# Performance work log

Measured on AMD Instinct MI355X. Metric: run time of the kernel, lower is better.

## Reference

```python
import jax, jax.numpy as jnp
import numpy as np

K = 1.0            # curvature (manifold.k); sqrt(K)=1 simplifies formulas
EPS = 1e-5         # module eps used in variance rescale
MIN_NORM = 1e-8    # clamp for sqrt of Lorentz inners
MAX_EUCLID = 10.0  # rescale_to_max_euclid cap (keeps cosh/sinh in fp32 range)


def l_inner(x, y):
    # Lorentz inner product <x,y>_L = -x0*y0 + <x_s, y_s>, keepdim
    return -x[..., :1] * y[..., :1] + jnp.sum(x[..., 1:] * y[..., 1:], axis=-1, keepdims=True)


def centroid(x):
    # Lorentzian centroid over the group axis (dim=-2)
    avg = jnp.mean(x, axis=-2, keepdims=True)
    denom = jnp.sqrt(jnp.clip(-l_inner(avg, avg), MIN_NORM, None))
    return avg / denom


def logmap(x, y):
    alpha = jnp.clip(-l_inner(x, y), 1.0 + 1e-7, None)   # -<x,y>_L >= 1
    dist = jnp.arccosh(alpha)
    nomin = y - alpha * x                                # y + <x,y>_L * x
    denom = jnp.sqrt(jnp.clip(l_inner(nomin, nomin), MIN_NORM, None))
    return dist * nomin / denom


def _plus_origin(p):
    # p + o where o = (1, 0, ..., 0)
    return jnp.concatenate([p[..., :1] + 1.0, p[..., 1:]], axis=-1)


def transp0back(x, v):
    # parallel transport of tangent v at x back to the origin o
    nom = -v[..., :1]                 # <o, v>_L = -v0
    denom = 1.0 + x[..., :1]          # K - <x, o>_L = 1 + x0
    return v + (nom / denom) * _plus_origin(x)


def transp0(y, v):
    # parallel transport of tangent v at origin o to point y
    nom = l_inner(y, v)
    denom = 1.0 + y[..., :1]          # K - <o, y>_L = 1 + y0
    return v + (nom / denom) * _plus_origin(y)


def rescale_to_max_euclid(u):
    n = jnp.linalg.norm(u, axis=-1, keepdims=True)
    scale = jnp.minimum(1.0, MAX_EUCLID / jnp.clip(n, MIN_NORM, None))
    return u * scale


def expmap(x, u):
    nrm = jnp.sqrt(jnp.clip(l_inner(u, u), MIN_NORM, None))
    return jnp.cosh(nrm) * x + jnp.sinh(nrm) * (u / nrm)


def setup_inputs() -> dict:
    key = jax.random.key(0)
    k1, = jax.random.split(key, 1)
    bs, h, w, c = 64, 56, 56, 128
    # sample spatial components, lift onto the hyperboloid: x0 = sqrt(1+|xs|^2)
    xs = 0.5 * jax.random.normal(k1, (bs, h, w, c - 1), dtype=jnp.float32)
    x0 = jnp.sqrt(1.0 + jnp.sum(xs * xs, axis=-1, keepdims=True))
    x = jnp.concatenate([x0, xs], axis=-1)
    gamma = jnp.ones((c,), dtype=jnp.float32)
    # beta = manifold.origin(c) = (1, 0, ..., 0)
    beta = jnp.zeros((c,), dtype=jnp.float32).at[0].set(1.0)
    return {"x": x, "gamma": gamma, "beta": beta, "groups": 8}


def reference(x, gamma, beta, groups):
    bs, h, w, c = x.shape
    xg = x.reshape(bs, -1, groups, c)                    # (bs, hw/g, g, c)
    mean = centroid(xg)                                  # (bs, hw/g, 1, c)
    x_T = logmap(mean, xg)                               # tangent at mean
    x_T = transp0back(mean, x_T)                         # tangent at origin
    # Frechet-style variance: mean Euclidean norm over spatial dim (dim=1)
    var = jnp.mean(jnp.linalg.norm(x_T, axis=-1, keepdims=True), axis=1, keepdims=True)
    x_T = x_T * (gamma / (var + EPS))
    x_T = rescale_to_max_euclid(x_T)
    x_T = transp0(beta, x_T)                             # transport to beta
    out = expmap(beta, x_T)
    return out.reshape(bs, h, w, c)
```

## Files before the change

### kernel.cpp

```cpp
#include <hip/hip_runtime.h>
#include <math.h>


constexpr int S_GROUPS = 392;
constexpr int N_GROUPS = 64 * S_GROUPS;

__device__ __forceinline__ void wave_lds_fence() {
  __asm__ volatile("" ::: "memory");
  __builtin_amdgcn_wave_barrier();
  __asm__ volatile("" ::: "memory");
}

__device__ __forceinline__ void rsum8x3(float& a, float& b, float& c) {
#pragma unroll
  for (int m = 1; m <= 4; m <<= 1) {
    a += __shfl_xor(a, m, 64);
    b += __shfl_xor(b, m, 64);
    c += __shfl_xor(c, m, 64);
  }
}

__device__ __forceinline__ void fold_mean(const float v[16], int lane,
                                          float& c0, float& c1) {
  float a8[8];
  const bool h5 = (lane & 32) != 0;
#pragma unroll
  for (int i = 0; i < 8; ++i) {
    float kp = h5 ? v[i + 8] : v[i];
    float sd = h5 ? v[i] : v[i + 8];
    a8[i] = kp + __shfl_xor(sd, 32, 64);
  }
  float a4[4];
  const bool h4 = (lane & 16) != 0;
#pragma unroll
  for (int i = 0; i < 4; ++i) {
    float kp = h4 ? a8[i + 4] : a8[i];
    float sd = h4 ? a8[i] : a8[i + 4];
    a4[i] = kp + __shfl_xor(sd, 16, 64);
  }
  const bool h3 = (lane & 8) != 0;
  float kp0 = h3 ? a4[2] : a4[0], sd0 = h3 ? a4[0] : a4[2];
  float kp1 = h3 ? a4[3] : a4[1], sd1 = h3 ? a4[1] : a4[3];
  c0 = (kp0 + __shfl_xor(sd0, 8, 64)) * 0.125f;
  c1 = (kp1 + __shfl_xor(sd1, 8, 64)) * 0.125f;
}

struct CoreOut {
  float avg[16];
  float sc, k, coef;
  float iaL, dpL, yyE, y0p, avg0;
};

__device__ __forceinline__ void core(const float v[16], int lane,
                                     float* __restrict__ smrow, CoreOut& o) {
  const int p = lane >> 3, q = lane & 7;
  float c0, c1;
  fold_mean(v, lane, c0, c1);
  *reinterpret_cast<float2*>(&smrow[q * 16 + p * 2]) = make_float2(c0, c1);
  wave_lds_fence();
#pragma unroll
  for (int j = 0; j < 4; ++j)
    *reinterpret_cast<float4*>(&o.avg[4 * j]) =
        *reinterpret_cast<const float4*>(&smrow[q * 16 + 4 * j]);
  wave_lds_fence();

  float pa = 0.f, pd = 0.f, py = 0.f;
#pragma unroll
  for (int i = 0; i < 16; ++i) {
    pa = fmaf(o.avg[i], o.avg[i], pa);
    pd = fmaf(o.avg[i], v[i], pd);
    py = fmaf(v[i], v[i], py);
  }
  if (q == 0) {
    pa -= 2.f * o.avg[0] * o.avg[0];
    pd -= 2.f * o.avg[0] * v[0];
  }
  rsum8x3(pa, pd, py);
  o.iaL = pa;
  o.dpL = pd;
  o.yyE = py;
  o.y0p = __shfl(v[0], lane & 56, 64);
  o.avg0 = __shfl(o.avg[0], 0, 64);

  float rden = rsqrtf(fmaxf(-pa, 1e-8f));
  float a_raw = -pd * rden;
  float alpha = fmaxf(a_raw, 1.f + 1e-7f);
  float t = alpha - 1.f;
  float dist = log1pf(t + sqrtf(t * (alpha + 1.f)));
  float yyL = py - 2.f * o.y0p * o.y0p;
  float inn = fmaxf(yyL + 2.f * alpha * a_raw - alpha * alpha, 1e-8f);
  o.sc = dist * rsqrtf(inn);
  float am = alpha * rden;
  float mean0 = rden * o.avg0;
  float v0 = o.sc * (o.y0p - am * o.avg0);
  o.coef = -v0 / (1.f + mean0);
  o.k = o.coef * rden - o.sc * am;
}

__device__ __forceinline__ float xt_norm(const CoreOut& A) {
  float yavgE = A.dpL + 2.f * A.avg0 * A.y0p;
  float aaE = A.iaL + 2.f * A.avg0 * A.avg0;
  float nsq = A.sc * A.sc * A.yyE + A.k * A.k * aaE + 2.f * A.sc * A.k * yavgE +
              A.coef * A.coef + 2.f * A.coef * (A.sc * A.y0p + A.k * A.avg0);
  return sqrtf(fmaxf(nsq, 0.f));
}

__global__ __launch_bounds__(256) void lngn_pass1(const float* __restrict__ x,
                                                  float* __restrict__ var_part) {
  __shared__ float sm[4][2][128];
  const int w = threadIdx.x >> 6, lane = threadIdx.x & 63;
  const int p = lane >> 3, q = lane & 7;
  const int wid0 = (blockIdx.x * 4 + w) * 2;
  const float* b0 = x + (size_t)wid0 * 1024 + p * 128 + q * 16;
  float vA[16], vB[16];
#pragma unroll
  for (int j = 0; j < 4; ++j) {
    *reinterpret_cast<float4*>(&vA[4 * j]) =
        *reinterpret_cast<const float4*>(b0 + 4 * j);
    *reinterpret_cast<float4*>(&vB[4 * j]) =
        *reinterpret_cast<const float4*>(b0 + 1024 + 4 * j);
  }
  CoreOut A, B;
  core(vA, lane, sm[w][0], A);
  core(vB, lane, sm[w][1], B);
  float nA = xt_norm(A), nB = xt_norm(B);
  if (q == 0) {
    var_part[(size_t)wid0 * 8 + p] = nA;
    var_part[(size_t)(wid0 + 1) * 8 + p] = nB;
  }
}

__global__ __launch_bounds__(256) void lngn_finalize(
    const float* __restrict__ var_part, float* __restrict__ var_out) {
  const int wv = (int)((blockIdx.x * 256 + threadIdx.x) >> 6);
  const int lane = threadIdx.x & 63;
  const int b = wv >> 3, p = wv & 7;
  const float* base = var_part + (size_t)b * S_GROUPS * 8 + p;
  float s = 0.f;
  for (int s0 = lane; s0 < S_GROUPS; s0 += 64) s += base[(size_t)s0 * 8];
#pragma unroll
  for (int m = 32; m >= 1; m >>= 1) s += __shfl_xor(s, m, 64);
  if (lane == 0) var_out[wv] = s * (1.f / (float)S_GROUPS);
}

__global__ __launch_bounds__(256) void lngn_pass2(
    const float* __restrict__ x, const float* __restrict__ gamma,
    const float* __restrict__ beta, const float* __restrict__ var,
    float* __restrict__ out) {
  __shared__ float sm[4][128];
  const int w = threadIdx.x >> 6, lane = threadIdx.x & 63;
  const int p = lane >> 3, q = lane & 7;
  const int wid = blockIdx.x * 4 + w;
  const size_t base = (size_t)wid * 1024 + p * 128 + q * 16;
  float v[16];
#pragma unroll
  for (int j = 0; j < 4; ++j)
    *reinterpret_cast<float4*>(&v[4 * j]) =
        *reinterpret_cast<const float4*>(x + base + 4 * j);
  CoreOut C;
  core(v, lane, sm[w], C);

  const int b = wid / S_GROUPS;
  const float s1 = 1.f / (var[b * 8 + p] + 1e-5f);
  float gm[16], bt[16];
#pragma unroll
  for (int j = 0; j < 4; ++j) {
    *reinterpret_cast<float4*>(&gm[4 * j]) =
        *reinterpret_cast<const float4*>(gamma + q * 16 + 4 * j);
    *reinterpret_cast<float4*>(&bt[4 * j]) =
        *reinterpret_cast<const float4*>(beta + q * 16 + 4 * j);
  }

  float u[16];
  float pe = 0.f, pb = 0.f, pbb = 0.f;
#pragma unroll
  for (int i = 0; i < 16; ++i) {
    float xt = fmaf(C.sc, v[i], C.k * C.avg[i]);
    if (i == 0) xt += (q == 0) ? C.coef : 0.f;
    u[i] = xt * (gm[i] * s1);
    pe = fmaf(u[i], u[i], pe);
    pb = fmaf(bt[i], u[i], pb);
    pbb = fmaf(bt[i], bt[i], pbb);
  }
  if (q == 0) {
    pb -= 2.f * bt[0] * u[0];
    pbb -= 2.f * bt[0] * bt[0];
  }
  rsum8x3(pe, pb, pbb);
  const float u0 = __shfl(u[0], 0, 64);
  const float bt0 = __shfl(bt[0], 0, 64);

  float n = sqrtf(pe);
  float scl = fminf(1.f, 10.f / fmaxf(n, 1e-8f));
  float c2 = scl * pb / (1.f + bt0);
  float uuL = pe - 2.f * u0 * u0;
  float innw = scl * scl * uuL + 2.f * scl * c2 * (pb - u0) +
               c2 * c2 * (pbb - 2.f * bt0 - 1.f);
  float nrm = sqrtf(fmaxf(innw, 1e-8f));
  float e = expf(nrm), ie = 1.f / e;
  float chv = 0.5f * (e + ie);
  float isn = (0.5f * (e - ie)) / nrm;
  float C1 = chv + isn * c2, C2 = isn * scl, C3 = isn * c2;
  float o16[16];
#pragma unroll
  for (int i = 0; i < 16; ++i) o16[i] = fmaf(C1, bt[i], C2 * u[i]);
  if (q == 0) o16[0] += C3;
  float* ob = out + base;
#pragma unroll
  for (int j = 0; j < 4; ++j)
    *reinterpret_cast<float4*>(ob + 4 * j) =
        *reinterpret_cast<const float4*>(&o16[4 * j]);
}

extern "C" void kernel_launch(void* const* d_in, const int* in_sizes, int n_in,
                              void* d_out, int out_size, void* d_ws,
                              size_t ws_size, hipStream_t stream) {
  const float* x = (const float*)d_in[0];
  const float* gamma = (const float*)d_in[1];
  const float* beta = (const float*)d_in[2];
  float* out = (float*)d_out;
  float* var_part = (float*)d_ws;
  float* var_final = var_part + (size_t)N_GROUPS * 8;

  lngn_pass1<<<N_GROUPS / 8, 256, 0, stream>>>(x, var_part);
  lngn_finalize<<<128, 256, 0, stream>>>(var_part, var_final);
  lngn_pass2<<<N_GROUPS / 4, 256, 0, stream>>>(x, gamma, beta, var_final, out);
}
```

Measured before the change: 224.4 us.

## Cache per-group centroid and coefficients in pass 1; fold variance reduction into pass 2

Pass 1 now writes each group's centroid vector and per-row logmap/transport scalars to workspace, and pre-sums pairs of row norms. The separate finalize kernel is removed: pass 2 reduces the variance partials itself, then loops over four groups per wave, reusing the cached centroid and scalars instead of recomputing the centroid, logmap and transport. This drops a launch and the duplicated core math. In exchange it adds workspace writes and reads, and every wave repeats the variance reduction (196 partials per row).

```diff
diff --git a/kernel.cpp b/kernel.cpp
--- a/kernel.cpp
+++ b/kernel.cpp
@@ -4,6 +4,7 @@
 
 constexpr int S_GROUPS = 392;
 constexpr int N_GROUPS = 64 * S_GROUPS;
+constexpr int PART = S_GROUPS / 2;
 
 __device__ __forceinline__ void wave_lds_fence() {
   __asm__ volatile("" ::: "memory");
@@ -11,6 +12,20 @@
   __asm__ volatile("" ::: "memory");
 }
 
+__device__ __forceinline__ void load16(float d[16], const float* __restrict__ s) {
+#pragma unroll
+  for (int j = 0; j < 4; ++j)
+    *reinterpret_cast<float4*>(&d[4 * j]) =
+        *reinterpret_cast<const float4*>(s + 4 * j);
+}
+
+__device__ __forceinline__ void store16(float* __restrict__ d, const float s[16]) {
+#pragma unroll
+  for (int j = 0; j < 4; ++j)
+    *reinterpret_cast<float4*>(d + 4 * j) =
+        *reinterpret_cast<const float4*>(&s[4 * j]);
+}
+
 __device__ __forceinline__ void rsum8x3(float& a, float& b, float& c) {
 #pragma unroll
   for (int m = 1; m <= 4; m <<= 1) {
@@ -18,6 +33,20 @@
     b += __shfl_xor(b, m, 64);
     c += __shfl_xor(c, m, 64);
   }
+}
+
+__device__ __forceinline__ void rsum8x2(float& a, float& b) {
+#pragma unroll
+  for (int m = 1; m <= 4; m <<= 1) {
+    a += __shfl_xor(a, m, 64);
+    b += __shfl_xor(b, m, 64);
+  }
+}
+
+__device__ __forceinline__ float rsum8(float a) {
+#pragma unroll
+  for (int m = 1; m <= 4; m <<= 1) a += __shfl_xor(a, m, 64);
+  return a;
 }
 
 __device__ __forceinline__ void fold_mean(const float v[16], int lane,
@@ -105,111 +134,109 @@
   return sqrtf(fmaxf(nsq, 0.f));
 }
 
-__global__ __launch_bounds__(256) void lngn_pass1(const float* __restrict__ x,
-                                                  float* __restrict__ var_part) {
+__global__ __launch_bounds__(256) void lngn_k1(const float* __restrict__ x,
+                                               float* __restrict__ var_part,
+                                               float* __restrict__ scal,
+                                               float* __restrict__ avg_ws) {
   __shared__ float sm[4][2][128];
   const int w = threadIdx.x >> 6, lane = threadIdx.x & 63;
   const int p = lane >> 3, q = lane & 7;
-  const int wid0 = (blockIdx.x * 4 + w) * 2;
-  const float* b0 = x + (size_t)wid0 * 1024 + p * 128 + q * 16;
+  const int off = p * 128 + q * 16;
+  const int wid = blockIdx.x * 4 + w;
+  const int g0 = wid * 2;
+  const float* b0 = x + (size_t)g0 * 1024 + off;
   float vA[16], vB[16];
-#pragma unroll
-  for (int j = 0; j < 4; ++j) {
-    *reinterpret_cast<float4*>(&vA[4 * j]) =
-        *reinterpret_cast<const float4*>(b0 + 4 * j);
-    *reinterpret_cast<float4*>(&vB[4 * j]) =
-        *reinterpret_cast<const float4*>(b0 + 1024 + 4 * j);
-  }
+  load16(vA, b0);
+  load16(vB, b0 + 1024);
   CoreOut A, B;
   core(vA, lane, sm[w][0], A);
   core(vB, lane, sm[w][1], B);
-  float nA = xt_norm(A), nB = xt_norm(B);
   if (q == 0) {
-    var_part[(size_t)wid0 * 8 + p] = nA;
-    var_part[(size_t)(wid0 + 1) * 8 + p] = nB;
-  }
-}
-
-__global__ __launch_bounds__(256) void lngn_finalize(
-    const float* __restrict__ var_part, float* __restrict__ var_out) {
-  const int wv = (int)((blockIdx.x * 256 + threadIdx.x) >> 6);
-  const int lane = threadIdx.x & 63;
-  const int b = wv >> 3, p = wv & 7;
-  const float* base = var_part + (size_t)b * S_GROUPS * 8 + p;
-  float s = 0.f;
-  for (int s0 = lane; s0 < S_GROUPS; s0 += 64) s += base[(size_t)s0 * 8];
-#pragma unroll
-  for (int m = 32; m >= 1; m >>= 1) s += __shfl_xor(s, m, 64);
-  if (lane == 0) var_out[wv] = s * (1.f / (float)S_GROUPS);
-}
-
-__global__ __launch_bounds__(256) void lngn_pass2(
+    *reinterpret_cast<float4*>(&scal[((size_t)g0 * 8 + p) * 4]) =
+        make_float4(A.sc, A.k, A.coef, 0.f);
+    *reinterpret_cast<float4*>(&scal[((size_t)(g0 + 1) * 8 + p) * 4]) =
+        make_float4(B.sc, B.k, B.coef, 0.f);
+    var_part[(size_t)wid * 8 + p] = xt_norm(A) + xt_norm(B);
+  }
+  if (p == 0) {
+    store16(avg_ws + (size_t)g0 * 128 + q * 16, A.avg);
+    store16(avg_ws + (size_t)(g0 + 1) * 128 + q * 16, B.avg);
+  }
+}
+
+__global__ __launch_bounds__(256) void lngn_k2(
     const float* __restrict__ x, const float* __restrict__ gamma,
-    const float* __restrict__ beta, const float* __restrict__ var,
+    const float* __restrict__ beta, const float* __restrict__ var_part,
+    const float* __restrict__ scal, const float* __restrict__ avg_ws,
     float* __restrict__ out) {
-  __shared__ float sm[4][128];
   const int w = threadIdx.x >> 6, lane = threadIdx.x & 63;
   const int p = lane >> 3, q = lane & 7;
+  const int off = p * 128 + q * 16;
   const int wid = blockIdx.x * 4 + w;
-  const size_t base = (size_t)wid * 1024 + p * 128 + q * 16;
+  const int b = wid / 98;
+
+  float vs = 0.f;
+  const float* vp = var_part + (size_t)b * PART * 8 + p;
+  for (int s = q; s < PART; s += 8) vs += vp[(size_t)s * 8];
+  vs = rsum8(vs);
+  const float s1 = 1.f / (vs * (1.f / (float)S_GROUPS) + 1e-5f);
+
+  float gm[16], bt[16];
+  load16(gm, gamma + q * 16);
+  load16(bt, beta + q * 16);
+  float pbb = 0.f;
+#pragma unroll
+  for (int i = 0; i < 16; ++i) pbb = fmaf(bt[i], bt[i], pbb);
+  if (q == 0) pbb -= 2.f * bt[0] * bt[0];
+  const float pbbL = rsum8(pbb);
+  const float bt0 = __shfl(bt[0], 0, 64);
+  const float kk = pbbL - 2.f * bt0 - 1.f;
+  const float ibt = 1.f / (1.f + bt0);
+
+  size_t g = (size_t)wid * 4;
   float v[16];
-#pragma unroll
-  for (int j = 0; j < 4; ++j)
-    *reinterpret_cast<float4*>(&v[4 * j]) =
-        *reinterpret_cast<const float4*>(x + base + 4 * j);
-  CoreOut C;
-  core(v, lane, sm[w], C);
-
-  const int b = wid / S_GROUPS;
-  const float s1 = 1.f / (var[b * 8 + p] + 1e-5f);
-  float gm[16], bt[16];
-#pragma unroll
-  for (int j = 0; j < 4; ++j) {
-    *reinterpret_cast<float4*>(&gm[4 * j]) =
-        *reinterpret_cast<const float4*>(gamma + q * 16 + 4 * j);
-    *reinterpret_cast<float4*>(&bt[4 * j]) =
-        *reinterpret_cast<const float4*>(beta + q * 16 + 4 * j);
-  }
-
-  float u[16];
-  float pe = 0.f, pb = 0.f, pbb = 0.f;
-#pragma unroll
-  for (int i = 0; i < 16; ++i) {
-    float xt = fmaf(C.sc, v[i], C.k * C.avg[i]);
-    if (i == 0) xt += (q == 0) ? C.coef : 0.f;
-    u[i] = xt * (gm[i] * s1);
-    pe = fmaf(u[i], u[i], pe);
-    pb = fmaf(bt[i], u[i], pb);
-    pbb = fmaf(bt[i], bt[i], pbb);
-  }
-  if (q == 0) {
-    pb -= 2.f * bt[0] * u[0];
-    pbb -= 2.f * bt[0] * bt[0];
-  }
-  rsum8x3(pe, pb, pbb);
-  const float u0 = __shfl(u[0], 0, 64);
-  const float bt0 = __shfl(bt[0], 0, 64);
-
-  float n = sqrtf(pe);
-  float scl = fminf(1.f, 10.f / fmaxf(n, 1e-8f));
-  float c2 = scl * pb / (1.f + bt0);
-  float uuL = pe - 2.f * u0 * u0;
-  float innw = scl * scl * uuL + 2.f * scl * c2 * (pb - u0) +
-               c2 * c2 * (pbb - 2.f * bt0 - 1.f);
-  float nrm = sqrtf(fmaxf(innw, 1e-8f));
-  float e = expf(nrm), ie = 1.f / e;
-  float chv = 0.5f * (e + ie);
-  float isn = (0.5f * (e - ie)) / nrm;
-  float C1 = chv + isn * c2, C2 = isn * scl, C3 = isn * c2;
-  float o16[16];
-#pragma unroll
-  for (int i = 0; i < 16; ++i) o16[i] = fmaf(C1, bt[i], C2 * u[i]);
-  if (q == 0) o16[0] += C3;
-  float* ob = out + base;
-#pragma unroll
-  for (int j = 0; j < 4; ++j)
-    *reinterpret_cast<float4*>(ob + 4 * j) =
-        *reinterpret_cast<const float4*>(&o16[4 * j]);
+  load16(v, x + g * 1024 + off);
+  for (int it = 0; it < 4; ++it) {
+    float vn[16];
+    if (it < 3) load16(vn, x + (g + 1) * 1024 + off);
+    float av[16];
+    load16(av, avg_ws + g * 128 + q * 16);
+    const float4 sck =
+        *reinterpret_cast<const float4*>(&scal[(g * 8 + p) * 4]);
+
+    float u[16];
+    float pe = 0.f, pb = 0.f;
+#pragma unroll
+    for (int i = 0; i < 16; ++i) {
+      float xt = fmaf(sck.x, v[i], sck.y * av[i]);
+      if (i == 0) xt += (q == 0) ? sck.z : 0.f;
+      u[i] = xt * (gm[i] * s1);
+      pe = fmaf(u[i], u[i], pe);
+      pb = fmaf(bt[i], u[i], pb);
+    }
+    if (q == 0) pb -= 2.f * bt[0] * u[0];
+    rsum8x2(pe, pb);
+
+    float n = sqrtf(pe);
+    float scl = fminf(1.f, 10.f / fmaxf(n, 1e-8f));
+    float c2 = scl * pb * ibt;
+    float innw = scl * scl * pe + 2.f * scl * c2 * pb + c2 * c2 * kk;
+    float nrm = sqrtf(fmaxf(innw, 1e-8f));
+    float e = expf(nrm), ie = 1.f / e;
+    float chv = 0.5f * (e + ie);
+    float isn = (0.5f * (e - ie)) / nrm;
+    float C1 = chv + isn * c2, C2 = isn * scl, C3 = isn * c2;
+#pragma unroll
+    for (int i = 0; i < 16; ++i) u[i] = fmaf(C1, bt[i], C2 * u[i]);
+    if (q == 0) u[0] += C3;
+    store16(out + g * 1024 + off, u);
+
+    if (it < 3) {
+#pragma unroll
+      for (int i = 0; i < 16; ++i) v[i] = vn[i];
+    }
+    ++g;
+  }
 }
 
 extern "C" void kernel_launch(void* const* d_in, const int* in_sizes, int n_in,
@@ -219,10 +246,12 @@
   const float* gamma = (const float*)d_in[1];
   const float* beta = (const float*)d_in[2];
   float* out = (float*)d_out;
+
   float* var_part = (float*)d_ws;
-  float* var_final = var_part + (size_t)N_GROUPS * 8;
-
-  lngn_pass1<<<N_GROUPS / 8, 256, 0, stream>>>(x, var_part);
-  lngn_finalize<<<128, 256, 0, stream>>>(var_part, var_final);
-  lngn_pass2<<<N_GROUPS / 4, 256, 0, stream>>>(x, gamma, beta, var_final, out);
-}
+  float* scal = var_part + (size_t)(N_GROUPS / 2) * 8;
+  float* avg_ws = scal + (size_t)N_GROUPS * 32;
+
+  lngn_k1<<<N_GROUPS / 8, 256, 0, stream>>>(x, var_part, scal, avg_ws);
+  lngn_k2<<<N_GROUPS / 16, 256, 0, stream>>>(x, gamma, beta, var_part, scal,
+                                             avg_ws, out);
+}
```

Result: slower. 236.6 us (+5.5%).
